# Kernel tuning notes

Hardware: AMD Instinct MI355X
Metric: run time of the kernel (lower is better)

## Reference

```python
import jax, jax.numpy as jnp
import numpy as np

N_CLUSTER = 5      # prototypes per class (init arg n_cluster)
NUM_CLASSES = 6    # hard-coded by `i // (len(prototypes)//6)` in the torch source


def setup_inputs() -> dict:
    key = jax.random.key(0)
    k0, k1, k2, k3 = jax.random.split(key, 4)
    B, C, H, W = 8, 256, 128, 128
    P = NUM_CLASSES * N_CLUSTER  # 30
    return {
        "assp_features": jax.random.normal(k0, (B, C, H, W), jnp.float32),
        "prototypes": jax.random.normal(k1, (P, B, C), jnp.float32),
        # key 1x1 conv == linear over channels: weight [128, C], bias [128]
        "Wk": jax.random.normal(k2, (128, C), jnp.float32) * 0.05,
        "bk": jnp.zeros((128,), jnp.float32),
        # one query 1x1 conv per class: [num_classes, 128, C] / [num_classes, 128]
        "Wq": jax.random.normal(k3, (NUM_CLASSES, 128, C), jnp.float32) * 0.05,
        "bq": jnp.zeros((NUM_CLASSES, 128), jnp.float32),
    }


def reference(assp_features, prototypes, Wk, bk, Wq, bq):
    B, C, H, W = assp_features.shape
    P = prototypes.shape[0]
    G = P // NUM_CLASSES  # prototypes sharing each class query

    # key: 1x1 conv -> [B, 128, H*W]
    key_out = jnp.einsum('bchw,kc->bkhw', assp_features, Wk) + bk[None, :, None, None]
    key_flat = key_out.reshape(B, 128, H * W)

    # queries: prototype i uses query_{i // G}; batch all P projections at once
    proto_g = prototypes.reshape(NUM_CLASSES, G, B, C)
    q = jnp.einsum('gpbc,gkc->gpbk', proto_g, Wq) + bq[:, None, None, :]
    q = q.reshape(P, B, 128)  # prototypesOut stacked: [P, B, 128]

    # similarity: bmm([B,1,128],[B,128,HW]) per prototype -> [B, P, H, W]
    sim = jnp.einsum('pbk,bkn->bpn', q, key_flat).reshape(B, P, H, W)

    # softmax(sim / P * n_cluster) over prototype axis, then max over prototypes
    w = jax.nn.softmax(sim * (N_CLUSTER / P), axis=1)
    w = jnp.max(w, axis=1)  # [B, H, W]

    assp_weighted = assp_features * w[:, None, :, :]
    return (assp_weighted, q, sim)
```

## Files before the change

### kernel.cpp

```cpp
#include <hip/hip_runtime.h>

#define BB    8
#define CC    256
#define HWN   16384
#define PP    30
#define PPAD  32
#define KD    128
#define GG    5
#define XsS   66
#define OFF_Q   (33554432u)
#define OFF_SIM (OFF_Q + 30720u)

typedef float  f32x4 __attribute__((ext_vector_type(4)));
typedef short  short8 __attribute__((ext_vector_type(8)));

static __device__ __forceinline__ unsigned short f2bf(float f) {
    unsigned u = __float_as_uint(f);
    u += 0x7fffu + ((u >> 16) & 1u);
    return (unsigned short)(u >> 16);
}

__global__ __launch_bounds__(256) void proj_kernel(
    const float* __restrict__ proto,
    const float* __restrict__ Wq,
    const float* __restrict__ bq,
    const float* __restrict__ Wk,
    const float* __restrict__ bk,
    float* __restrict__ qout,
    short* __restrict__ Afrag,
    float* __restrict__ c0)
{
    const int pb = blockIdx.x;
    const int p = pb / BB, b = pb % BB;
    const int tid = threadIdx.x;

    const int kb = tid >> 5, sub = (tid >> 3) & 3, j = tid & 7;
    const int lane = (p & 15) + 16 * sub;
    const size_t fidx = (((size_t)(b * 2 + (p >> 4)) * 8 + kb) * 64 + lane) * 8 + j;

    if (p >= PP) {
        Afrag[fidx] = 0;
        if (tid == 0) c0[b * PPAD + p] = -1e30f;
        return;
    }
    const int g = p / GG;

    __shared__ float ps[CC];
    __shared__ float qs[KD];

    for (int c = tid; c < CC; c += 256)
        ps[c] = proto[(size_t)(p * BB + b) * CC + c];
    __syncthreads();

    if (tid < KD) {
        const float* wrow = Wq + (size_t)(g * KD + tid) * CC;
        float a = 0.f;
        #pragma unroll 4
        for (int c = 0; c < CC; ++c) a += ps[c] * wrow[c];
        a += bq[g * KD + tid];
        qout[(size_t)(p * BB + b) * KD + tid] = a;
        qs[tid] = a;
    }
    __syncthreads();

    float a = 0.f;
    #pragma unroll 4
    for (int k = 0; k < KD; ++k) a += qs[k] * Wk[k * CC + tid];
    Afrag[fidx] = (short)f2bf(a);

    if (tid == 0) {
        float s = 0.f;
        for (int k = 0; k < KD; ++k) s += qs[k] * bk[k];
        c0[b * PPAD + p] = s;
    }
}

__global__ __launch_bounds__(256) void fused_kernel(
    const float* __restrict__ X,
    const short* __restrict__ Afrag,
    const float* __restrict__ c0,
    float* __restrict__ out0,
    float* __restrict__ sim)
{
    const int b    = blockIdx.y;
    const int tid  = threadIdx.x;
    const int lane = tid & 63;
    const int wid  = tid >> 6;
    const int col  = lane & 15;
    const int kgrp = lane >> 4;
    const int n0   = blockIdx.x * 64;

    __shared__ unsigned short Xs[CC * XsS];
    __shared__ float c0s[PPAD];
    __shared__ float wbuf[64];

    if (tid < PPAD) c0s[tid] = c0[b * PPAD + tid];

    {
        const float* gb = X + (size_t)b * CC * HWN + n0;
        #pragma unroll
        for (int it = 0; it < 4; ++it) {
            f32x4 v[4];
            #pragma unroll
            for (int u = 0; u < 4; ++u) {
                const int flat = (it * 4 + u) * 256 + tid;
                const int ch = flat >> 4, pq = flat & 15;
                v[u] = *(const f32x4*)(gb + (size_t)ch * HWN + pq * 4);
            }
            #pragma unroll
            for (int u = 0; u < 4; ++u) {
                const int flat = (it * 4 + u) * 256 + tid;
                const int ch = flat >> 4, pq = flat & 15;
                const unsigned lo = (unsigned)f2bf(v[u].x) | ((unsigned)f2bf(v[u].y) << 16);
                const unsigned hi = (unsigned)f2bf(v[u].z) | ((unsigned)f2bf(v[u].w) << 16);
                unsigned* dst = (unsigned*)&Xs[ch * XsS + pq * 4];
                dst[0] = lo;
                dst[1] = hi;
            }
        }
    }
    __syncthreads();

    const short8* af8 = (const short8*)Afrag;
    const size_t afbase = (size_t)b * 2 * 8 * 64;

    f32x4 accA = {}, accB = {};
    #pragma unroll 2
    for (int kb = 0; kb < 8; ++kb) {
        const short8 afA = af8[afbase + (size_t)kb * 64 + lane];
        const short8 afB = af8[afbase + (size_t)(8 + kb) * 64 + lane];
        short8 bfr;
        #pragma unroll
        for (int j = 0; j < 8; ++j)
            bfr[j] = (short)Xs[(kb * 32 + kgrp * 8 + j) * XsS + wid * 16 + col];
        accA = __builtin_amdgcn_mfma_f32_16x16x32_bf16(afA, bfr, accA, 0, 0, 0);
        accB = __builtin_amdgcn_mfma_f32_16x16x32_bf16(afB, bfr, accB, 0, 0, 0);
    }

    const int nw = n0 + wid * 16;
    float v[8];
    float pm = -1e30f;
    #pragma unroll
    for (int r = 0; r < 4; ++r) {
        const int row = kgrp * 4 + r;
        const float tA = accA[r] + c0s[row];
        const float tB = accB[r] + c0s[row + 16];
        v[r] = tA;
        v[r + 4] = tB;
        pm = fmaxf(pm, fmaxf(tA, tB));
        __builtin_nontemporal_store(tA,
            sim + ((size_t)b * PP + row) * HWN + nw + col);
        if (row + 16 < PP)
            __builtin_nontemporal_store(tB,
                sim + ((size_t)b * PP + row + 16) * HWN + nw + col);
    }
    float m = pm;
    m = fmaxf(m, __shfl_xor(m, 16));
    m = fmaxf(m, __shfl_xor(m, 32));

    float s = 0.f;
    #pragma unroll
    for (int r = 0; r < 8; ++r)
        s += __expf((v[r] - m) * (1.f / 6.f));
    s += __shfl_xor(s, 16);
    s += __shfl_xor(s, 32);

    if (lane < 16) wbuf[wid * 16 + lane] = 1.f / s;
    __syncthreads();

    const int pq = tid & 15, cg = tid >> 4;
    const f32x4 w4 = *(const f32x4*)(&wbuf[pq * 4]);
    float* ob = out0 + (size_t)b * CC * HWN + n0 + pq * 4;
    #pragma unroll 4
    for (int i = 0; i < 16; ++i) {
        const int ch = cg * 16 + i;
        const unsigned* src = (const unsigned*)&Xs[ch * XsS + pq * 4];
        const unsigned lo = src[0], hi = src[1];
        f32x4 x;
        x.x = __uint_as_float(lo << 16);
        x.y = __uint_as_float(lo & 0xffff0000u);
        x.z = __uint_as_float(hi << 16);
        x.w = __uint_as_float(hi & 0xffff0000u);
        __builtin_nontemporal_store(x * w4, (f32x4*)(ob + (size_t)ch * HWN));
    }
}

extern "C" void kernel_launch(void* const* d_in, const int* in_sizes, int n_in,
                              void* d_out, int out_size, void* d_ws, size_t ws_size,
                              hipStream_t stream) {
    const float* X     = (const float*)d_in[0];
    const float* proto = (const float*)d_in[1];
    const float* Wk    = (const float*)d_in[2];
    const float* bk    = (const float*)d_in[3];
    const float* Wq    = (const float*)d_in[4];
    const float* bq    = (const float*)d_in[5];

    float* out  = (float*)d_out;
    float* qout = out + OFF_Q;
    float* sim  = out + OFF_SIM;

    short* Afrag = (short*)d_ws;
    float* c0    = (float*)(Afrag + BB * 2 * 8 * 64 * 8);

    proj_kernel<<<PPAD * BB, 256, 0, stream>>>(proto, Wq, bq, Wk, bk, qout, Afrag, c0);

    dim3 grid(HWN / 64, BB);
    fused_kernel<<<grid, 256, 0, stream>>>(X, Afrag, c0, out, sim);
}
```

Measured before the change: 69.00 us.

## Process two 64-column tiles per block and prefetch the next X tile into registers

Each block now covers 128 spatial columns as two 64-column tiles. All 16 loads of the second tile are issued into registers before the first tile's weighted output is written, so global reads overlap the store phase. The grid is halved, and each thread holds 16 float4 registers, which raises register pressure and may lower occupancy. Extra block barriers are added between the two tiles.

```diff
diff --git a/kernel.cpp b/kernel.cpp
--- a/kernel.cpp
+++ b/kernel.cpp
@@ -88,7 +88,7 @@
     const int wid  = tid >> 6;
     const int col  = lane & 15;
     const int kgrp = lane >> 4;
-    const int n0   = blockIdx.x * 64;
+    const int t0   = blockIdx.x * 128;
 
     __shared__ unsigned short Xs[CC * XsS];
     __shared__ float c0s[PPAD];
@@ -96,92 +96,115 @@
 
     if (tid < PPAD) c0s[tid] = c0[b * PPAD + tid];
 
+    const int ch_s = tid >> 4;
+    const int pq_s = tid & 15;
+
+    f32x4 L[16];
     {
-        const float* gb = X + (size_t)b * CC * HWN + n0;
+        const float* gb = X + (size_t)b * CC * HWN + t0;
         #pragma unroll
-        for (int it = 0; it < 4; ++it) {
-            f32x4 v[4];
+        for (int it = 0; it < 16; ++it)
+            L[it] = *(const f32x4*)(gb + (size_t)(it * 16 + ch_s) * HWN + pq_s * 4);
+    }
+    #pragma unroll
+    for (int it = 0; it < 16; ++it) {
+        const int ch = it * 16 + ch_s;
+        const unsigned lo = (unsigned)f2bf(L[it].x) | ((unsigned)f2bf(L[it].y) << 16);
+        const unsigned hi = (unsigned)f2bf(L[it].z) | ((unsigned)f2bf(L[it].w) << 16);
+        unsigned* dst = (unsigned*)&Xs[ch * XsS + pq_s * 4];
+        dst[0] = lo;
+        dst[1] = hi;
+    }
+    __syncthreads();
+
+    const short8* af8 = (const short8*)Afrag;
+    const size_t afbase = (size_t)b * 2 * 8 * 64;
+
+    #pragma unroll
+    for (int t = 0; t < 2; ++t) {
+        const int n0 = t0 + t * 64;
+
+        f32x4 accA = {}, accB = {};
+        #pragma unroll 2
+        for (int kb = 0; kb < 8; ++kb) {
+            const short8 afA = af8[afbase + (size_t)kb * 64 + lane];
+            const short8 afB = af8[afbase + (size_t)(8 + kb) * 64 + lane];
+            short8 bfr;
             #pragma unroll
-            for (int u = 0; u < 4; ++u) {
-                const int flat = (it * 4 + u) * 256 + tid;
-                const int ch = flat >> 4, pq = flat & 15;
-                v[u] = *(const f32x4*)(gb + (size_t)ch * HWN + pq * 4);
+            for (int j = 0; j < 8; ++j)
+                bfr[j] = (short)Xs[(kb * 32 + kgrp * 8 + j) * XsS + wid * 16 + col];
+            accA = __builtin_amdgcn_mfma_f32_16x16x32_bf16(afA, bfr, accA, 0, 0, 0);
+            accB = __builtin_amdgcn_mfma_f32_16x16x32_bf16(afB, bfr, accB, 0, 0, 0);
+        }
+
+        const int nw = n0 + wid * 16;
+        float v[8];
+        float pm = -1e30f;
+        #pragma unroll
+        for (int r = 0; r < 4; ++r) {
+            const int row = kgrp * 4 + r;
+            const float tA = accA[r] + c0s[row];
+            const float tB = accB[r] + c0s[row + 16];
+            v[r] = tA;
+            v[r + 4] = tB;
+            pm = fmaxf(pm, fmaxf(tA, tB));
+            __builtin_nontemporal_store(tA,
+                sim + ((size_t)b * PP + row) * HWN + nw + col);
+            if (row + 16 < PP)
+                __builtin_nontemporal_store(tB,
+                    sim + ((size_t)b * PP + row + 16) * HWN + nw + col);
+        }
+        float m = pm;
+        m = fmaxf(m, __shfl_xor(m, 16));
+        m = fmaxf(m, __shfl_xor(m, 32));
+
+        float s = 0.f;
+        #pragma unroll
+        for (int r = 0; r < 8; ++r)
+            s += __expf((v[r] - m) * (1.f / 6.f));
+        s += __shfl_xor(s, 16);
+        s += __shfl_xor(s, 32);
+
+        if (lane < 16) wbuf[wid * 16 + lane] = 1.f / s;
+        __syncthreads();
+
+        if (t == 0) {
+            const float* gb = X + (size_t)b * CC * HWN + t0 + 64;
+            #pragma unroll
+            for (int it = 0; it < 16; ++it)
+                L[it] = *(const f32x4*)(gb + (size_t)(it * 16 + ch_s) * HWN + pq_s * 4);
+        }
+
+        {
+            const f32x4 w4 = *(const f32x4*)(&wbuf[pq_s * 4]);
+            float* ob = out0 + (size_t)b * CC * HWN + n0 + pq_s * 4;
+            #pragma unroll 4
+            for (int i = 0; i < 16; ++i) {
+                const int ch = ch_s * 16 + i;
+                const unsigned* src = (const unsigned*)&Xs[ch * XsS + pq_s * 4];
+                const unsigned lo = src[0], hi = src[1];
+                f32x4 x;
+                x.x = __uint_as_float(lo << 16);
+                x.y = __uint_as_float(lo & 0xffff0000u);
+                x.z = __uint_as_float(hi << 16);
+                x.w = __uint_as_float(hi & 0xffff0000u);
+                __builtin_nontemporal_store(x * w4, (f32x4*)(ob + (size_t)ch * HWN));
             }
+        }
+
+        if (t == 0) {
+            __syncthreads();
             #pragma unroll
-            for (int u = 0; u < 4; ++u) {
-                const int flat = (it * 4 + u) * 256 + tid;
-                const int ch = flat >> 4, pq = flat & 15;
-                const unsigned lo = (unsigned)f2bf(v[u].x) | ((unsigned)f2bf(v[u].y) << 16);
-                const unsigned hi = (unsigned)f2bf(v[u].z) | ((unsigned)f2bf(v[u].w) << 16);
-                unsigned* dst = (unsigned*)&Xs[ch * XsS + pq * 4];
+            for (int it = 0; it < 16; ++it) {
+                const int ch = it * 16 + ch_s;
+                const unsigned lo = (unsigned)f2bf(L[it].x) | ((unsigned)f2bf(L[it].y) << 16);
+                const unsigned hi = (unsigned)f2bf(L[it].z) | ((unsigned)f2bf(L[it].w) << 16);
+                unsigned* dst = (unsigned*)&Xs[ch * XsS + pq_s * 4];
                 dst[0] = lo;
                 dst[1] = hi;
             }
-        }
-    }
-    __syncthreads();
-
-    const short8* af8 = (const short8*)Afrag;
-    const size_t afbase = (size_t)b * 2 * 8 * 64;
-
-    f32x4 accA = {}, accB = {};
-    #pragma unroll 2
-    for (int kb = 0; kb < 8; ++kb) {
-        const short8 afA = af8[afbase + (size_t)kb * 64 + lane];
-        const short8 afB = af8[afbase + (size_t)(8 + kb) * 64 + lane];
-        short8 bfr;
-        #pragma unroll
-        for (int j = 0; j < 8; ++j)
-            bfr[j] = (short)Xs[(kb * 32 + kgrp * 8 + j) * XsS + wid * 16 + col];
-        accA = __builtin_amdgcn_mfma_f32_16x16x32_bf16(afA, bfr, accA, 0, 0, 0);
-        accB = __builtin_amdgcn_mfma_f32_16x16x32_bf16(afB, bfr, accB, 0, 0, 0);
-    }
-
-    const int nw = n0 + wid * 16;
-    float v[8];
-    float pm = -1e30f;
-    #pragma unroll
-    for (int r = 0; r < 4; ++r) {
-        const int row = kgrp * 4 + r;
-        const float tA = accA[r] + c0s[row];
-        const float tB = accB[r] + c0s[row + 16];
-        v[r] = tA;
-        v[r + 4] = tB;
-        pm = fmaxf(pm, fmaxf(tA, tB));
-        __builtin_nontemporal_store(tA,
-            sim + ((size_t)b * PP + row) * HWN + nw + col);
-        if (row + 16 < PP)
-            __builtin_nontemporal_store(tB,
-                sim + ((size_t)b * PP + row + 16) * HWN + nw + col);
-    }
-    float m = pm;
-    m = fmaxf(m, __shfl_xor(m, 16));
-    m = fmaxf(m, __shfl_xor(m, 32));
-
-    float s = 0.f;
-    #pragma unroll
-    for (int r = 0; r < 8; ++r)
-        s += __expf((v[r] - m) * (1.f / 6.f));
-    s += __shfl_xor(s, 16);
-    s += __shfl_xor(s, 32);
-
-    if (lane < 16) wbuf[wid * 16 + lane] = 1.f / s;
-    __syncthreads();
-
-    const int pq = tid & 15, cg = tid >> 4;
-    const f32x4 w4 = *(const f32x4*)(&wbuf[pq * 4]);
-    float* ob = out0 + (size_t)b * CC * HWN + n0 + pq * 4;
-    #pragma unroll 4
-    for (int i = 0; i < 16; ++i) {
-        const int ch = cg * 16 + i;
-        const unsigned* src = (const unsigned*)&Xs[ch * XsS + pq * 4];
-        const unsigned lo = src[0], hi = src[1];
-        f32x4 x;
-        x.x = __uint_as_float(lo << 16);
-        x.y = __uint_as_float(lo & 0xffff0000u);
-        x.z = __uint_as_float(hi << 16);
-        x.w = __uint_as_float(hi & 0xffff0000u);
-        __builtin_nontemporal_store(x * w4, (f32x4*)(ob + (size_t)ch * HWN));
+            __syncthreads();
+        }
     }
 }
 
@@ -204,6 +227,6 @@
 
     proj_kernel<<<PPAD * BB, 256, 0, stream>>>(proto, Wq, bq, Wk, bk, qout, Afrag, c0);
 
-    dim3 grid(HWN / 64, BB);
+    dim3 grid(HWN / 128, BB);
     fused_kernel<<<grid, 256, 0, stream>>>(X, Afrag, c0, out, sim);
 }
```

Result: no change. 69.71 us (+1.0%).

## Halve fused kernel tile to 32 pixels with 128 threads and preload A fragments

Applied to the files above, without the earlier changes.

The fused kernel now handles 32 pixels per block with two waves instead of 64 pixels with four. This halves the LDS tile, so more blocks can be resident per CU, and the grid doubles. All bf16 A fragments for the batch are preloaded into registers before the X tile is staged, so their global loads overlap the X loads and leave the MFMA loop. The cost is higher register pressure and twice as many blocks, each reloading the same A fragments.

```diff
diff --git a/kernel.cpp b/kernel.cpp
--- a/kernel.cpp
+++ b/kernel.cpp
@@ -7,7 +7,7 @@
 #define PPAD  32
 #define KD    128
 #define GG    5
-#define XsS   66
+#define XsS   34
 #define OFF_Q   (33554432u)
 #define OFF_SIM (OFF_Q + 30720u)
 
@@ -75,7 +75,7 @@
     }
 }
 
-__global__ __launch_bounds__(256) void fused_kernel(
+__global__ __launch_bounds__(128, 4) void fused_kernel(
     const float* __restrict__ X,
     const short* __restrict__ Afrag,
     const float* __restrict__ c0,
@@ -85,17 +85,29 @@
     const int b    = blockIdx.y;
     const int tid  = threadIdx.x;
     const int lane = tid & 63;
-    const int wid  = tid >> 6;
+    const int w    = tid >> 6;
     const int col  = lane & 15;
     const int kgrp = lane >> 4;
-    const int n0   = blockIdx.x * 64;
+    const int n0   = blockIdx.x * 32;
+    const int nw   = n0 + w * 16;
 
     __shared__ unsigned short Xs[CC * XsS];
     __shared__ float c0s[PPAD];
-    __shared__ float wbuf[64];
+    __shared__ float wbuf[32];
 
     if (tid < PPAD) c0s[tid] = c0[b * PPAD + tid];
 
+    const short8* af8 = (const short8*)Afrag;
+    const size_t afbase = (size_t)b * 2 * 8 * 64;
+    short8 afA[8], afB[8];
+    #pragma unroll
+    for (int kb = 0; kb < 8; ++kb) {
+        afA[kb] = af8[afbase + (size_t)kb * 64 + lane];
+        afB[kb] = af8[afbase + (size_t)(8 + kb) * 64 + lane];
+    }
+
+    const int ch_s = tid >> 3;
+    const int pq_s = tid & 7;
     {
         const float* gb = X + (size_t)b * CC * HWN + n0;
         #pragma unroll
@@ -103,17 +115,15 @@
             f32x4 v[4];
             #pragma unroll
             for (int u = 0; u < 4; ++u) {
-                const int flat = (it * 4 + u) * 256 + tid;
-                const int ch = flat >> 4, pq = flat & 15;
-                v[u] = *(const f32x4*)(gb + (size_t)ch * HWN + pq * 4);
+                const int ch = (it * 4 + u) * 16 + ch_s;
+                v[u] = *(const f32x4*)(gb + (size_t)ch * HWN + pq_s * 4);
             }
             #pragma unroll
             for (int u = 0; u < 4; ++u) {
-                const int flat = (it * 4 + u) * 256 + tid;
-                const int ch = flat >> 4, pq = flat & 15;
+                const int ch = (it * 4 + u) * 16 + ch_s;
                 const unsigned lo = (unsigned)f2bf(v[u].x) | ((unsigned)f2bf(v[u].y) << 16);
                 const unsigned hi = (unsigned)f2bf(v[u].z) | ((unsigned)f2bf(v[u].w) << 16);
-                unsigned* dst = (unsigned*)&Xs[ch * XsS + pq * 4];
+                unsigned* dst = (unsigned*)&Xs[ch * XsS + pq_s * 4];
                 dst[0] = lo;
                 dst[1] = hi;
             }
@@ -121,23 +131,17 @@
     }
     __syncthreads();
 
-    const short8* af8 = (const short8*)Afrag;
-    const size_t afbase = (size_t)b * 2 * 8 * 64;
-
     f32x4 accA = {}, accB = {};
-    #pragma unroll 2
+    #pragma unroll
     for (int kb = 0; kb < 8; ++kb) {
-        const short8 afA = af8[afbase + (size_t)kb * 64 + lane];
-        const short8 afB = af8[afbase + (size_t)(8 + kb) * 64 + lane];
         short8 bfr;
         #pragma unroll
         for (int j = 0; j < 8; ++j)
-            bfr[j] = (short)Xs[(kb * 32 + kgrp * 8 + j) * XsS + wid * 16 + col];
-        accA = __builtin_amdgcn_mfma_f32_16x16x32_bf16(afA, bfr, accA, 0, 0, 0);
-        accB = __builtin_amdgcn_mfma_f32_16x16x32_bf16(afB, bfr, accB, 0, 0, 0);
-    }
-
-    const int nw = n0 + wid * 16;
+            bfr[j] = (short)Xs[(kb * 32 + kgrp * 8 + j) * XsS + w * 16 + col];
+        accA = __builtin_amdgcn_mfma_f32_16x16x32_bf16(afA[kb], bfr, accA, 0, 0, 0);
+        accB = __builtin_amdgcn_mfma_f32_16x16x32_bf16(afB[kb], bfr, accB, 0, 0, 0);
+    }
+
     float v[8];
     float pm = -1e30f;
     #pragma unroll
@@ -165,16 +169,15 @@
     s += __shfl_xor(s, 16);
     s += __shfl_xor(s, 32);
 
-    if (lane < 16) wbuf[wid * 16 + lane] = 1.f / s;
-    __syncthreads();
-
-    const int pq = tid & 15, cg = tid >> 4;
-    const f32x4 w4 = *(const f32x4*)(&wbuf[pq * 4]);
-    float* ob = out0 + (size_t)b * CC * HWN + n0 + pq * 4;
+    if (lane < 16) wbuf[w * 16 + lane] = 1.f / s;
+    __syncthreads();
+
+    const f32x4 w4 = *(const f32x4*)(&wbuf[pq_s * 4]);
+    float* ob = out0 + (size_t)b * CC * HWN + n0 + pq_s * 4;
     #pragma unroll 4
     for (int i = 0; i < 16; ++i) {
-        const int ch = cg * 16 + i;
-        const unsigned* src = (const unsigned*)&Xs[ch * XsS + pq * 4];
+        const int ch = ch_s * 16 + i;
+        const unsigned* src = (const unsigned*)&Xs[ch * XsS + pq_s * 4];
         const unsigned lo = src[0], hi = src[1];
         f32x4 x;
         x.x = __uint_as_float(lo << 16);
@@ -204,6 +207,6 @@
 
     proj_kernel<<<PPAD * BB, 256, 0, stream>>>(proto, Wq, bq, Wk, bk, qout, Afrag, c0);
 
-    dim3 grid(HWN / 64, BB);
-    fused_kernel<<<grid, 256, 0, stream>>>(X, Afrag, c0, out, sim);
-}
+    dim3 grid(HWN / 32, BB);
+    fused_kernel<<<grid, 128, 0, stream>>>(X, Afrag, c0, out, sim);
+}
```

New measurement: 67.58 us, median of 2. 1.02x faster.
